# Optimization experiments

Measured on AMD Instinct MI355X. Metric: run time of the kernel, lower is better.

The kernel has to match this reference:

```python
import jax, jax.numpy as jnp
import numpy as np

N_NODES = 100000
N_EDGES = 3200000
NFEAT = 256
NHID = 256
NCLASS = 64


def setup_inputs() -> dict:
    key = jax.random.key(0)
    ks = jax.random.split(key, 12)
    x = jax.random.normal(ks[0], (N_NODES, NFEAT), dtype=jnp.float32)
    edge_src = jax.random.randint(ks[1], (N_EDGES,), 0, N_NODES, dtype=jnp.int32)
    edge_dst = jnp.sort(jax.random.randint(ks[2], (N_EDGES,), 0, N_NODES, dtype=jnp.int32))
    edge_w = jax.random.uniform(ks[3], (N_EDGES,), dtype=jnp.float32)
    s1 = 1.0 / np.sqrt(NFEAT)
    s2 = 1.0 / np.sqrt(NHID)
    W1 = jax.random.normal(ks[4], (NFEAT, NHID), dtype=jnp.float32) * s1
    b1 = jnp.zeros((NHID,), dtype=jnp.float32)
    W2 = jax.random.normal(ks[5], (NHID, NHID), dtype=jnp.float32) * s2
    b2 = jnp.zeros((NHID,), dtype=jnp.float32)
    WL1 = jax.random.normal(ks[6], (NHID, NCLASS), dtype=jnp.float32) * s2
    bL1 = jnp.zeros((NCLASS,), dtype=jnp.float32)
    WL2 = jax.random.normal(ks[7], (NHID, NCLASS), dtype=jnp.float32) * s2
    bL2 = jnp.zeros((NCLASS,), dtype=jnp.float32)
    return {"x": x, "edge_src": edge_src, "edge_dst": edge_dst, "edge_w": edge_w,
            "W1": W1, "b1": b1, "W2": W2, "b2": b2,
            "WL1": WL1, "bL1": bL1, "WL2": WL2, "bL2": bL2}


def reference(x, edge_src, edge_dst, edge_w, W1, b1, W2, b2, WL1, bL1, WL2, bL2):
    n = x.shape[0]

    def spmm(h):
        # adj @ h with adj given as (src, dst, w) edge list:
        # out[dst] += w * h[src]
        return jax.ops.segment_sum(edge_w[:, None] * h[edge_src], edge_dst, num_segments=n)

    # GraphConvolution layer 1: support = x @ W; out = adj @ support + b; relu
    # (dropout inactive in eval mode)
    h = jax.nn.relu(spmm(x @ W1) + b1)
    # GraphConvolution layer 2
    h = jax.nn.relu(spmm(h @ W2) + b2)
    # twin dense heads
    logit1 = h @ WL1 + bL1
    logit2 = h @ WL2 + bL2
    return (logit1, logit2)
```

## Files before the change

kernel.cpp:

```cpp
#include <hip/hip_runtime.h>
#include <hip/hip_bf16.h>
#include <type_traits>

typedef __attribute__((ext_vector_type(8))) short short8;
typedef __attribute__((ext_vector_type(4))) float f32x4;
typedef __attribute__((ext_vector_type(2))) float f32x2;

__device__ inline unsigned short f2bf(float f) {
    union { float f; unsigned int u; } x; x.f = f;
    return (unsigned short)((x.u + 0x7fffu + ((x.u >> 16) & 1u)) >> 16);
}
__device__ inline float bflo(unsigned int u) { return __uint_as_float(u << 16); }
__device__ inline float bfhi(unsigned int u) { return __uint_as_float(u & 0xffff0000u); }

__global__ void rowptr_kernel(const int* __restrict__ dst, int* __restrict__ rp,
                              int E, int N) {
    int e = blockIdx.x * blockDim.x + threadIdx.x;
    if (e >= E) return;
    int d1 = dst[e];
    int d0 = (e == 0) ? -1 : dst[e - 1];
    for (int n = d0 + 1; n <= d1; n++) rp[n] = e;
    if (e <= N) {
        int dlast = dst[E - 1];
        if (e > dlast) rp[e] = E;
    }
}

__global__ void prep_kernel(const float* __restrict__ W1, const float* __restrict__ W2,
                            const float* __restrict__ WL1, const float* __restrict__ WL2,
                            unsigned short* __restrict__ W1t, unsigned short* __restrict__ W2t,
                            unsigned short* __restrict__ WLt) {
    int b = blockIdx.x, k = threadIdx.x;
    if (b < 256) {
        W1t[(size_t)b * 256 + k] = f2bf(W1[(size_t)k * 256 + b]);
    } else if (b < 512) {
        int n = b - 256;
        W2t[(size_t)n * 256 + k] = f2bf(W2[(size_t)k * 256 + n]);
    } else {
        int c = b - 512;
        float v = (c < 64) ? WL1[(size_t)k * 64 + c] : WL2[(size_t)k * 64 + (c - 64)];
        WLt[(size_t)c * 256 + k] = f2bf(v);
    }
}

template <typename AT, typename OT>
__global__ __launch_bounds__(256) void gemm_kernel(
    const AT* __restrict__ A, const unsigned short* __restrict__ Bt,
    OT* __restrict__ C, int M)
{
    __shared__ __align__(16) unsigned short As[128][40];
    __shared__ __align__(16) unsigned short Bs[128][40];
    const int t = threadIdx.x;
    const int row0 = blockIdx.y * 128;
    const int col0 = blockIdx.x * 128;
    const int wid = t >> 6, lane = t & 63;
    const int wm = (wid >> 1) * 64, wn = (wid & 1) * 64;
    const int qk = (lane >> 4) * 8, r16 = lane & 15;

    f32x4 acc[4][4];
#pragma unroll
    for (int i = 0; i < 4; i++)
#pragma unroll
        for (int j = 0; j < 4; j++) acc[i][j] = (f32x4){0.f, 0.f, 0.f, 0.f};

    for (int k0 = 0; k0 < 256; k0 += 32) {
#pragma unroll
        for (int i = 0; i < 2; i++) {
            int ch = t + i * 256;
            int m = ch >> 2;
            int ko = (ch & 3) * 8;
            int row = row0 + m;
            uint4 pk;
            if (row < M) {
                if constexpr (std::is_same<AT, float>::value) {
                    const uint4* p = (const uint4*)(A + (size_t)row * 256 + k0 + ko);
                    uint4 u = p[0], v = p[1];
                    pk.x = ((u.x + 0x8000u) >> 16) | ((u.y + 0x8000u) & 0xffff0000u);
                    pk.y = ((u.z + 0x8000u) >> 16) | ((u.w + 0x8000u) & 0xffff0000u);
                    pk.z = ((v.x + 0x8000u) >> 16) | ((v.y + 0x8000u) & 0xffff0000u);
                    pk.w = ((v.z + 0x8000u) >> 16) | ((v.w + 0x8000u) & 0xffff0000u);
                } else {
                    pk = *(const uint4*)(A + (size_t)row * 256 + k0 + ko);
                }
            } else {
                pk = (uint4){0u, 0u, 0u, 0u};
            }
            *(uint4*)(&As[m][ko]) = pk;
            *(uint4*)(&Bs[m][ko]) = *(const uint4*)(Bt + (size_t)(col0 + m) * 256 + k0 + ko);
        }
        __syncthreads();
        short8 av[4], bv[4];
#pragma unroll
        for (int mt = 0; mt < 4; mt++) av[mt] = *(const short8*)(&As[wm + mt * 16 + r16][qk]);
#pragma unroll
        for (int nt = 0; nt < 4; nt++) bv[nt] = *(const short8*)(&Bs[wn + nt * 16 + r16][qk]);
#pragma unroll
        for (int mt = 0; mt < 4; mt++)
#pragma unroll
            for (int nt = 0; nt < 4; nt++)
                acc[mt][nt] = __builtin_amdgcn_mfma_f32_16x16x32_bf16(av[mt], bv[nt], acc[mt][nt], 0, 0, 0);
        __syncthreads();
    }
#pragma unroll
    for (int mt = 0; mt < 4; mt++) {
#pragma unroll
        for (int r = 0; r < 4; r++) {
            int row = row0 + wm + mt * 16 + (lane >> 4) * 4 + r;
            if (row >= M) continue;
#pragma unroll
            for (int nt = 0; nt < 4; nt++) {
                int col = col0 + wn + nt * 16 + r16;
                float v = acc[mt][nt][r];
                if constexpr (std::is_same<OT, unsigned char>::value) {
                    unsigned int p = (unsigned int)__builtin_amdgcn_cvt_pk_fp8_f32(v, v, 0, false);
                    C[(size_t)row * 256 + col] = (unsigned char)(p & 0xffu);
                } else {
                    C[(size_t)row * 256 + col] = f2bf(v);
                }
            }
        }
    }
}

__global__ __launch_bounds__(256) void head_kernel(
    const unsigned short* __restrict__ A, const unsigned short* __restrict__ Bt,
    const float* __restrict__ bL1, const float* __restrict__ bL2,
    float* __restrict__ out, int M)
{
    __shared__ __align__(16) unsigned short As[128][40];
    __shared__ __align__(16) unsigned short Bs[128][40];
    const int t = threadIdx.x;
    const int row0 = blockIdx.x * 128;
    const int wid = t >> 6, lane = t & 63;
    const int wm = (wid >> 1) * 64, wn = (wid & 1) * 64;
    const int qk = (lane >> 4) * 8, r16 = lane & 15;

    f32x4 acc[4][4];
#pragma unroll
    for (int i = 0; i < 4; i++)
#pragma unroll
        for (int j = 0; j < 4; j++) acc[i][j] = (f32x4){0.f, 0.f, 0.f, 0.f};

    for (int k0 = 0; k0 < 256; k0 += 32) {
#pragma unroll
        for (int i = 0; i < 2; i++) {
            int ch = t + i * 256;
            int m = ch >> 2;
            int ko = (ch & 3) * 8;
            int row = row0 + m;
            uint4 pk = (uint4){0u, 0u, 0u, 0u};
            if (row < M) pk = *(const uint4*)(A + (size_t)row * 256 + k0 + ko);
            *(uint4*)(&As[m][ko]) = pk;
            *(uint4*)(&Bs[m][ko]) = *(const uint4*)(Bt + (size_t)m * 256 + k0 + ko);
        }
        __syncthreads();
        short8 av[4], bv[4];
#pragma unroll
        for (int mt = 0; mt < 4; mt++) av[mt] = *(const short8*)(&As[wm + mt * 16 + r16][qk]);
#pragma unroll
        for (int nt = 0; nt < 4; nt++) bv[nt] = *(const short8*)(&Bs[wn + nt * 16 + r16][qk]);
#pragma unroll
        for (int mt = 0; mt < 4; mt++)
#pragma unroll
            for (int nt = 0; nt < 4; nt++)
                acc[mt][nt] = __builtin_amdgcn_mfma_f32_16x16x32_bf16(av[mt], bv[nt], acc[mt][nt], 0, 0, 0);
        __syncthreads();
    }
#pragma unroll
    for (int mt = 0; mt < 4; mt++) {
#pragma unroll
        for (int r = 0; r < 4; r++) {
            int row = row0 + wm + mt * 16 + (lane >> 4) * 4 + r;
            if (row >= M) continue;
#pragma unroll
            for (int nt = 0; nt < 4; nt++) {
                int col = wn + nt * 16 + r16;
                float v = acc[mt][nt][r];
                if (col < 64) {
                    out[(size_t)row * 64 + col] = v + bL1[col];
                } else {
                    out[(size_t)M * 64 + (size_t)row * 64 + (col - 64)] = v + bL2[col - 64];
                }
            }
        }
    }
}

__device__ inline void acc16f8(float* a, uint4 r, float w) {
    f32x2 p;
    p = __builtin_amdgcn_cvt_pk_f32_fp8((int)r.x, false); a[0]  += w * p.x; a[1]  += w * p.y;
    p = __builtin_amdgcn_cvt_pk_f32_fp8((int)r.x, true);  a[2]  += w * p.x; a[3]  += w * p.y;
    p = __builtin_amdgcn_cvt_pk_f32_fp8((int)r.y, false); a[4]  += w * p.x; a[5]  += w * p.y;
    p = __builtin_amdgcn_cvt_pk_f32_fp8((int)r.y, true);  a[6]  += w * p.x; a[7]  += w * p.y;
    p = __builtin_amdgcn_cvt_pk_f32_fp8((int)r.z, false); a[8]  += w * p.x; a[9]  += w * p.y;
    p = __builtin_amdgcn_cvt_pk_f32_fp8((int)r.z, true);  a[10] += w * p.x; a[11] += w * p.y;
    p = __builtin_amdgcn_cvt_pk_f32_fp8((int)r.w, false); a[12] += w * p.x; a[13] += w * p.y;
    p = __builtin_amdgcn_cvt_pk_f32_fp8((int)r.w, true);  a[14] += w * p.x; a[15] += w * p.y;
}

__global__ __launch_bounds__(256) void spmm_fp8_kernel(
    const unsigned char* __restrict__ sup, const int* __restrict__ rp,
    const int* __restrict__ esrc, const float* __restrict__ ew,
    const float* __restrict__ bias, unsigned short* __restrict__ out, int nnodes)
{
    const int wid = threadIdx.x >> 6, lane = threadIdx.x & 63;
    const int node = blockIdx.x * 4 + wid;
    if (node >= nnodes) return;
    const int g = lane >> 4;
    const int f16 = (lane & 15) * 16;
    const unsigned char* supf = sup + f16;
    const int beg = rp[node], end = rp[node + 1];

    float a[16];
#pragma unroll
    for (int i = 0; i < 16; i++) a[i] = 0.f;

    int e = beg;
    for (; e + 8 <= end; e += 8) {
        const int s0 = esrc[e + g],     s1 = esrc[e + 4 + g];
        const float w0 = ew[e + g],     w1 = ew[e + 4 + g];
        const uint4 r0 = *(const uint4*)(supf + (size_t)s0 * 256);
        const uint4 r1 = *(const uint4*)(supf + (size_t)s1 * 256);
        acc16f8(a, r0, w0);
        acc16f8(a, r1, w1);
    }
    for (; e + 4 <= end; e += 4) {
        const int s = esrc[e + g];
        const float w = ew[e + g];
        const uint4 r = *(const uint4*)(supf + (size_t)s * 256);
        acc16f8(a, r, w);
    }
    {
        const int rem = end - e;
        if (g < rem) {
            const int s = esrc[e + g];
            const float w = ew[e + g];
            const uint4 r = *(const uint4*)(supf + (size_t)s * 256);
            acc16f8(a, r, w);
        }
    }
#pragma unroll
    for (int i = 0; i < 16; i++) {
        a[i] += __shfl_xor(a[i], 16);
        a[i] += __shfl_xor(a[i], 32);
    }

    if (g == 0) {
        const float4 b0 = *(const float4*)(bias + f16);
        const float4 b1 = *(const float4*)(bias + f16 + 4);
        const float4 b2 = *(const float4*)(bias + f16 + 8);
        const float4 b3 = *(const float4*)(bias + f16 + 12);
        a[0] += b0.x; a[1] += b0.y; a[2]  += b0.z; a[3]  += b0.w;
        a[4] += b1.x; a[5] += b1.y; a[6]  += b1.z; a[7]  += b1.w;
        a[8] += b2.x; a[9] += b2.y; a[10] += b2.z; a[11] += b2.w;
        a[12] += b3.x; a[13] += b3.y; a[14] += b3.z; a[15] += b3.w;
#pragma unroll
        for (int i = 0; i < 16; i++) a[i] = a[i] > 0.f ? a[i] : 0.f;
        uint4 o0, o1;
        o0.x = (unsigned int)f2bf(a[0])  | ((unsigned int)f2bf(a[1])  << 16);
        o0.y = (unsigned int)f2bf(a[2])  | ((unsigned int)f2bf(a[3])  << 16);
        o0.z = (unsigned int)f2bf(a[4])  | ((unsigned int)f2bf(a[5])  << 16);
        o0.w = (unsigned int)f2bf(a[6])  | ((unsigned int)f2bf(a[7])  << 16);
        o1.x = (unsigned int)f2bf(a[8])  | ((unsigned int)f2bf(a[9])  << 16);
        o1.y = (unsigned int)f2bf(a[10]) | ((unsigned int)f2bf(a[11]) << 16);
        o1.z = (unsigned int)f2bf(a[12]) | ((unsigned int)f2bf(a[13]) << 16);
        o1.w = (unsigned int)f2bf(a[14]) | ((unsigned int)f2bf(a[15]) << 16);
        *(uint4*)(out + (size_t)node * 256 + f16) = o0;
        *(uint4*)(out + (size_t)node * 256 + f16 + 8) = o1;
    }
}

extern "C" void kernel_launch(void* const* d_in, const int* in_sizes, int n_in,
                              void* d_out, int out_size, void* d_ws, size_t ws_size,
                              hipStream_t stream) {
    const float* x    = (const float*)d_in[0];
    const int*   esrc = (const int*)d_in[1];
    const int*   edst = (const int*)d_in[2];
    const float* ew   = (const float*)d_in[3];
    const float* W1   = (const float*)d_in[4];
    const float* b1   = (const float*)d_in[5];
    const float* W2   = (const float*)d_in[6];
    const float* b2   = (const float*)d_in[7];
    const float* WL1  = (const float*)d_in[8];
    const float* bL1  = (const float*)d_in[9];
    const float* WL2  = (const float*)d_in[10];
    const float* bL2  = (const float*)d_in[11];
    float* out = (float*)d_out;

    const int N = in_sizes[0] / 256;
    const int E = in_sizes[1];

    char* ws = (char*)d_ws;
    size_t off = 0;
    auto alloc = [&](size_t bytes) -> void* {
        void* p = ws + off;
        off = (off + bytes + 511) & ~(size_t)511;
        return p;
    };
    int* rp              = (int*)alloc((size_t)(N + 1) * 4);
    unsigned short* W1t  = (unsigned short*)alloc((size_t)256 * 256 * 2);
    unsigned short* W2t  = (unsigned short*)alloc((size_t)256 * 256 * 2);
    unsigned short* WLt  = (unsigned short*)alloc((size_t)128 * 256 * 2);
    unsigned char* sup8  = (unsigned char*)alloc((size_t)N * 256);
    unsigned short* hbuf = (unsigned short*)alloc((size_t)N * 256 * 2);

    const int mblocks = (N + 127) / 128;

    rowptr_kernel<<<(E + 255) / 256, 256, 0, stream>>>(edst, rp, E, N);
    prep_kernel<<<640, 256, 0, stream>>>(W1, W2, WL1, WL2, W1t, W2t, WLt);

    gemm_kernel<float, unsigned char><<<dim3(2, mblocks), 256, 0, stream>>>(
        x, W1t, sup8, N);
    spmm_fp8_kernel<<<(N + 3) / 4, 256, 0, stream>>>(
        sup8, rp, esrc, ew, b1, hbuf, N);
    gemm_kernel<unsigned short, unsigned char><<<dim3(2, mblocks), 256, 0, stream>>>(
        hbuf, W2t, sup8, N);
    spmm_fp8_kernel<<<(N + 3) / 4, 256, 0, stream>>>(
        sup8, rp, esrc, ew, b2, hbuf, N);
    head_kernel<<<dim3(mblocks, 1), 256, 0, stream>>>(hbuf, WLt, bL1, bL2, out, N);
}
```

Baseline: 519.5 us.

## Use async global-to-LDS loads in GEMMs, pack fp8 stores with permuted columns

The GEMM and head kernels now stage tiles with global_load_lds direct-to-LDS 16-byte loads into unpadded shared arrays, replacing register-staged copies and the zero-fill branch with clamped row indices. The first-layer input is converted to bf16 by a separate pre-pass so one GEMM kernel serves both layers. The GEMM epilogue packs four fp8 values per 32-bit store, which permutes output columns. That permutation is compensated by reordering W2, the head weights and the biases with sg(). This adds an extra pass over x and relies on the unpadded LDS layout, which may cause bank conflicts.

```diff
diff --git a/kernel.cpp b/kernel.cpp
--- a/kernel.cpp
+++ b/kernel.cpp
@@ -1,6 +1,5 @@
 #include <hip/hip_runtime.h>
 #include <hip/hip_bf16.h>
-#include <type_traits>
 
 typedef __attribute__((ext_vector_type(8))) short short8;
 typedef __attribute__((ext_vector_type(4))) float f32x4;
@@ -10,8 +9,16 @@
     union { float f; unsigned int u; } x; x.f = f;
     return (unsigned short)((x.u + 0x7fffu + ((x.u >> 16) & 1u)) >> 16);
 }
-__device__ inline float bflo(unsigned int u) { return __uint_as_float(u << 16); }
-__device__ inline float bfhi(unsigned int u) { return __uint_as_float(u & 0xffff0000u); }
+
+#define ASYNC16(gptr, lptr)                                                      \
+    __builtin_amdgcn_global_load_lds(                                            \
+        (const __attribute__((address_space(1))) unsigned int*)(gptr),           \
+        (__attribute__((address_space(3))) unsigned int*)(lptr), 16, 0, 0)
+
+__device__ __host__ inline int sg(int j) {
+    int p = j & 63;
+    return (j & ~63) | ((p >> 2) + 16 * (p & 3));
+}
 
 __global__ void rowptr_kernel(const int* __restrict__ dst, int* __restrict__ rp,
                               int E, int N) {
@@ -26,30 +33,50 @@
     }
 }
 
+__global__ void x2bf_kernel(const float* __restrict__ x, unsigned short* __restrict__ xb,
+                            int n8) {
+    int i = blockIdx.x * blockDim.x + threadIdx.x;
+    if (i >= n8) return;
+    const uint4* p = (const uint4*)(x + (size_t)i * 8);
+    uint4 u = p[0], v = p[1];
+    uint4 pk;
+    pk.x = ((u.x + 0x8000u) >> 16) | ((u.y + 0x8000u) & 0xffff0000u);
+    pk.y = ((u.z + 0x8000u) >> 16) | ((u.w + 0x8000u) & 0xffff0000u);
+    pk.z = ((v.x + 0x8000u) >> 16) | ((v.y + 0x8000u) & 0xffff0000u);
+    pk.w = ((v.z + 0x8000u) >> 16) | ((v.w + 0x8000u) & 0xffff0000u);
+    *(uint4*)(xb + (size_t)i * 8) = pk;
+}
+
 __global__ void prep_kernel(const float* __restrict__ W1, const float* __restrict__ W2,
                             const float* __restrict__ WL1, const float* __restrict__ WL2,
+                            const float* __restrict__ b1, const float* __restrict__ b2,
                             unsigned short* __restrict__ W1t, unsigned short* __restrict__ W2t,
-                            unsigned short* __restrict__ WLt) {
+                            unsigned short* __restrict__ WLt,
+                            float* __restrict__ b1p, float* __restrict__ b2p) {
     int b = blockIdx.x, k = threadIdx.x;
     if (b < 256) {
         W1t[(size_t)b * 256 + k] = f2bf(W1[(size_t)k * 256 + b]);
     } else if (b < 512) {
         int n = b - 256;
-        W2t[(size_t)n * 256 + k] = f2bf(W2[(size_t)k * 256 + n]);
+        W2t[(size_t)n * 256 + k] = f2bf(W2[(size_t)sg(k) * 256 + n]);
+    } else if (b < 640) {
+        int c = b - 512;
+        int ks = sg(k);
+        float v = (c < 64) ? WL1[(size_t)ks * 64 + c] : WL2[(size_t)ks * 64 + (c - 64)];
+        WLt[(size_t)c * 256 + k] = f2bf(v);
+    } else if (b == 640) {
+        b1p[k] = b1[sg(k)];
     } else {
-        int c = b - 512;
-        float v = (c < 64) ? WL1[(size_t)k * 64 + c] : WL2[(size_t)k * 64 + (c - 64)];
-        WLt[(size_t)c * 256 + k] = f2bf(v);
-    }
-}
-
-template <typename AT, typename OT>
-__global__ __launch_bounds__(256) void gemm_kernel(
-    const AT* __restrict__ A, const unsigned short* __restrict__ Bt,
-    OT* __restrict__ C, int M)
+        b2p[k] = b2[sg(k)];
+    }
+}
+
+__global__ __launch_bounds__(256) void gemm_f8_kernel(
+    const unsigned short* __restrict__ A, const unsigned short* __restrict__ Bt,
+    unsigned char* __restrict__ C, int M)
 {
-    __shared__ __align__(16) unsigned short As[128][40];
-    __shared__ __align__(16) unsigned short Bs[128][40];
+    __shared__ __align__(16) unsigned short As[128 * 32];
+    __shared__ __align__(16) unsigned short Bs[128 * 32];
     const int t = threadIdx.x;
     const int row0 = blockIdx.y * 128;
     const int col0 = blockIdx.x * 128;
@@ -57,6 +84,12 @@
     const int wm = (wid >> 1) * 64, wn = (wid & 1) * 64;
     const int qk = (lane >> 4) * 8, r16 = lane & 15;
 
+    const int c0 = t, c1 = t + 256;
+    const int am0 = min(row0 + (c0 >> 2), M - 1);
+    const int am1 = min(row0 + (c1 >> 2), M - 1);
+    const int ak0 = (c0 & 3) * 8, ak1 = (c1 & 3) * 8;
+    const int bm0 = col0 + (c0 >> 2), bm1 = col0 + (c1 >> 2);
+
     f32x4 acc[4][4];
 #pragma unroll
     for (int i = 0; i < 4; i++)
@@ -64,36 +97,16 @@
         for (int j = 0; j < 4; j++) acc[i][j] = (f32x4){0.f, 0.f, 0.f, 0.f};
 
     for (int k0 = 0; k0 < 256; k0 += 32) {
-#pragma unroll
-        for (int i = 0; i < 2; i++) {
-            int ch = t + i * 256;
-            int m = ch >> 2;
-            int ko = (ch & 3) * 8;
-            int row = row0 + m;
-            uint4 pk;
-            if (row < M) {
-                if constexpr (std::is_same<AT, float>::value) {
-                    const uint4* p = (const uint4*)(A + (size_t)row * 256 + k0 + ko);
-                    uint4 u = p[0], v = p[1];
-                    pk.x = ((u.x + 0x8000u) >> 16) | ((u.y + 0x8000u) & 0xffff0000u);
-                    pk.y = ((u.z + 0x8000u) >> 16) | ((u.w + 0x8000u) & 0xffff0000u);
-                    pk.z = ((v.x + 0x8000u) >> 16) | ((v.y + 0x8000u) & 0xffff0000u);
-                    pk.w = ((v.z + 0x8000u) >> 16) | ((v.w + 0x8000u) & 0xffff0000u);
-                } else {
-                    pk = *(const uint4*)(A + (size_t)row * 256 + k0 + ko);
-                }
-            } else {
-                pk = (uint4){0u, 0u, 0u, 0u};
-            }
-            *(uint4*)(&As[m][ko]) = pk;
-            *(uint4*)(&Bs[m][ko]) = *(const uint4*)(Bt + (size_t)(col0 + m) * 256 + k0 + ko);
-        }
+        ASYNC16(A + (size_t)am0 * 256 + k0 + ak0, &As[c0 * 8]);
+        ASYNC16(A + (size_t)am1 * 256 + k0 + ak1, &As[c1 * 8]);
+        ASYNC16(Bt + (size_t)bm0 * 256 + k0 + ak0, &Bs[c0 * 8]);
+        ASYNC16(Bt + (size_t)bm1 * 256 + k0 + ak1, &Bs[c1 * 8]);
         __syncthreads();
         short8 av[4], bv[4];
 #pragma unroll
-        for (int mt = 0; mt < 4; mt++) av[mt] = *(const short8*)(&As[wm + mt * 16 + r16][qk]);
-#pragma unroll
-        for (int nt = 0; nt < 4; nt++) bv[nt] = *(const short8*)(&Bs[wn + nt * 16 + r16][qk]);
+        for (int mt = 0; mt < 4; mt++) av[mt] = *(const short8*)(&As[(wm + mt * 16 + r16) * 32 + qk]);
+#pragma unroll
+        for (int nt = 0; nt < 4; nt++) bv[nt] = *(const short8*)(&Bs[(wn + nt * 16 + r16) * 32 + qk]);
 #pragma unroll
         for (int mt = 0; mt < 4; mt++)
 #pragma unroll
@@ -103,21 +116,15 @@
     }
 #pragma unroll
     for (int mt = 0; mt < 4; mt++) {
+        const int rowb = row0 + wm + mt * 16 + (lane >> 4) * 4;
 #pragma unroll
         for (int r = 0; r < 4; r++) {
-            int row = row0 + wm + mt * 16 + (lane >> 4) * 4 + r;
+            const int row = rowb + r;
             if (row >= M) continue;
-#pragma unroll
-            for (int nt = 0; nt < 4; nt++) {
-                int col = col0 + wn + nt * 16 + r16;
-                float v = acc[mt][nt][r];
-                if constexpr (std::is_same<OT, unsigned char>::value) {
-                    unsigned int p = (unsigned int)__builtin_amdgcn_cvt_pk_fp8_f32(v, v, 0, false);
-                    C[(size_t)row * 256 + col] = (unsigned char)(p & 0xffu);
-                } else {
-                    C[(size_t)row * 256 + col] = f2bf(v);
-                }
-            }
+            int w = 0;
+            w = __builtin_amdgcn_cvt_pk_fp8_f32(acc[mt][0][r], acc[mt][1][r], w, false);
+            w = __builtin_amdgcn_cvt_pk_fp8_f32(acc[mt][2][r], acc[mt][3][r], w, true);
+            *(unsigned int*)(C + (size_t)row * 256 + col0 + wn + r16 * 4) = (unsigned int)w;
         }
     }
 }
@@ -127,14 +134,20 @@
     const float* __restrict__ bL1, const float* __restrict__ bL2,
     float* __restrict__ out, int M)
 {
-    __shared__ __align__(16) unsigned short As[128][40];
-    __shared__ __align__(16) unsigned short Bs[128][40];
+    __shared__ __align__(16) unsigned short As[128 * 32];
+    __shared__ __align__(16) unsigned short Bs[128 * 32];
     const int t = threadIdx.x;
     const int row0 = blockIdx.x * 128;
     const int wid = t >> 6, lane = t & 63;
     const int wm = (wid >> 1) * 64, wn = (wid & 1) * 64;
     const int qk = (lane >> 4) * 8, r16 = lane & 15;
 
+    const int c0 = t, c1 = t + 256;
+    const int am0 = min(row0 + (c0 >> 2), M - 1);
+    const int am1 = min(row0 + (c1 >> 2), M - 1);
+    const int ak0 = (c0 & 3) * 8, ak1 = (c1 & 3) * 8;
+    const int bm0 = c0 >> 2, bm1 = c1 >> 2;
+
     f32x4 acc[4][4];
 #pragma unroll
     for (int i = 0; i < 4; i++)
@@ -142,23 +155,16 @@
         for (int j = 0; j < 4; j++) acc[i][j] = (f32x4){0.f, 0.f, 0.f, 0.f};
 
     for (int k0 = 0; k0 < 256; k0 += 32) {
-#pragma unroll
-        for (int i = 0; i < 2; i++) {
-            int ch = t + i * 256;
-            int m = ch >> 2;
-            int ko = (ch & 3) * 8;
-            int row = row0 + m;
-            uint4 pk = (uint4){0u, 0u, 0u, 0u};
-            if (row < M) pk = *(const uint4*)(A + (size_t)row * 256 + k0 + ko);
-            *(uint4*)(&As[m][ko]) = pk;
-            *(uint4*)(&Bs[m][ko]) = *(const uint4*)(Bt + (size_t)m * 256 + k0 + ko);
-        }
+        ASYNC16(A + (size_t)am0 * 256 + k0 + ak0, &As[c0 * 8]);
+        ASYNC16(A + (size_t)am1 * 256 + k0 + ak1, &As[c1 * 8]);
+        ASYNC16(Bt + (size_t)bm0 * 256 + k0 + ak0, &Bs[c0 * 8]);
+        ASYNC16(Bt + (size_t)bm1 * 256 + k0 + ak1, &Bs[c1 * 8]);
         __syncthreads();
         short8 av[4], bv[4];
 #pragma unroll
-        for (int mt = 0; mt < 4; mt++) av[mt] = *(const short8*)(&As[wm + mt * 16 + r16][qk]);
-#pragma unroll
-        for (int nt = 0; nt < 4; nt++) bv[nt] = *(const short8*)(&Bs[wn + nt * 16 + r16][qk]);
+        for (int mt = 0; mt < 4; mt++) av[mt] = *(const short8*)(&As[(wm + mt * 16 + r16) * 32 + qk]);
+#pragma unroll
+        for (int nt = 0; nt < 4; nt++) bv[nt] = *(const short8*)(&Bs[(wn + nt * 16 + r16) * 32 + qk]);
 #pragma unroll
         for (int mt = 0; mt < 4; mt++)
 #pragma unroll
@@ -301,21 +307,20 @@
     unsigned short* W1t  = (unsigned short*)alloc((size_t)256 * 256 * 2);
     unsigned short* W2t  = (unsigned short*)alloc((size_t)256 * 256 * 2);
     unsigned short* WLt  = (unsigned short*)alloc((size_t)128 * 256 * 2);
+    float* b1p           = (float*)alloc(256 * 4);
+    float* b2p           = (float*)alloc(256 * 4);
     unsigned char* sup8  = (unsigned char*)alloc((size_t)N * 256);
     unsigned short* hbuf = (unsigned short*)alloc((size_t)N * 256 * 2);
 
     const int mblocks = (N + 127) / 128;
 
     rowptr_kernel<<<(E + 255) / 256, 256, 0, stream>>>(edst, rp, E, N);
-    prep_kernel<<<640, 256, 0, stream>>>(W1, W2, WL1, WL2, W1t, W2t, WLt);
-
-    gemm_kernel<float, unsigned char><<<dim3(2, mblocks), 256, 0, stream>>>(
-        x, W1t, sup8, N);
-    spmm_fp8_kernel<<<(N + 3) / 4, 256, 0, stream>>>(
-        sup8, rp, esrc, ew, b1, hbuf, N);
-    gemm_kernel<unsigned short, unsigned char><<<dim3(2, mblocks), 256, 0, stream>>>(
-        hbuf, W2t, sup8, N);
-    spmm_fp8_kernel<<<(N + 3) / 4, 256, 0, stream>>>(
-        sup8, rp, esrc, ew, b2, hbuf, N);
-    head_kernel<<<dim3(mblocks, 1), 256, 0, stream>>>(hbuf, WLt, bL1, bL2, out, N);
-}
+    x2bf_kernel<<<(N * 256 / 8 + 255) / 256, 256, 0, stream>>>(x, hbuf, N * 256 / 8);
+    prep_kernel<<<642, 256, 0, stream>>>(W1, W2, WL1, WL2, b1, b2, W1t, W2t, WLt, b1p, b2p);
+
+    gemm_f8_kernel<<<dim3(2, mblocks), 256, 0, stream>>>(hbuf, W1t, sup8, N);
+    spmm_fp8_kernel<<<(N + 3) / 4, 256, 0, stream>>>(sup8, rp, esrc, ew, b1p, hbuf, N);
+    gemm_f8_kernel<<<dim3(2, mblocks), 256, 0, stream>>>(hbuf, W2t, sup8, N);
+    spmm_fp8_kernel<<<(N + 3) / 4, 256, 0, stream>>>(sup8, rp, esrc, ew, b2p, hbuf, N);
+    head_kernel<<<mblocks, 256, 0, stream>>>(hbuf, WLt, bL1, bL2, out, N);
+}
```

Measured after the change: 497.3 us. 1.04x faster.
